# Optimization experiments

Hardware: AMD Instinct MI355X
Metric: run time of the kernel (lower is better)

The kernel has to match this reference:

```python
import jax, jax.numpy as jnp
import numpy as np

B, T, D, K = 4, 2048, 1024, 4

def setup_inputs() -> dict:
    key = jax.random.key(0)
    ks = jax.random.split(key, 4)
    u = jax.random.normal(ks[0], (B, T, D), dtype=jnp.float32)
    s0 = jnp.zeros((B, K, D), dtype=jnp.float32)
    W_in = jax.random.normal(ks[1], (K * D, D), dtype=jnp.float32) * (1.0 / np.sqrt(D))
    b_in = jnp.zeros((K * D,), dtype=jnp.float32)
    W_out = jax.random.normal(ks[2], (D, K * D), dtype=jnp.float32) * (1.0 / np.sqrt(K * D))
    b_out = jnp.zeros((D,), dtype=jnp.float32)
    decay_logit = jax.random.normal(ks[3], (K,), dtype=jnp.float32)
    return {"u": u, "s0": s0, "W_in": W_in, "b_in": b_in,
            "W_out": W_out, "b_out": b_out, "decay_logit": decay_logit}

def reference(u, s0, W_in, b_in, W_out, b_out, decay_logit):
    # u: (B,T,D); s0: (B,K,D)
    Bb, Tt, Dd = u.shape
    Kk = decay_logit.shape[0]
    # input projection -> (B,T,K,D) -> (T,B,K,D) for scan over time
    inp = (jnp.einsum('btd,ed->bte', u, W_in) + b_in).reshape(Bb, Tt, Kk, Dd)
    xs = jnp.transpose(inp, (1, 0, 2, 3))  # (T,B,K,D)
    decay = jax.nn.sigmoid(decay_logit).reshape(1, Kk, 1)  # (1,K,1)

    def step(s, x):
        s_next = decay * s + x
        return s_next, s_next

    s_last, s_seq = jax.lax.scan(step, s0, xs)  # s_seq: (T,B,K,D)
    g_in = jnp.transpose(s_seq, (1, 0, 2, 3)).reshape(Bb, Tt, Kk * Dd)
    g = jnp.einsum('bte,de->btd', g_in, W_out) + b_out
    return g, s_last
```

## Files before the change

kernel.cpp:

```cpp
#include <hip/hip_runtime.h>


#define Bb 4
#define Tt 2048
#define Dd 1024
#define Kk 4
#define BT (Bb*Tt)
#define Ee (Kk*Dd)
#define NCH 32
#define LCH 64

typedef __bf16 bf16x8 __attribute__((ext_vector_type(8)));
typedef float  f32x4  __attribute__((ext_vector_type(4)));

__device__ __forceinline__ float bf2f(ushort u){
  union { unsigned int i; float f; } x; x.i = ((unsigned int)u) << 16; return x.f;
}
__device__ __forceinline__ ushort f2bf(float f){
  union { unsigned int i; float f; } x; x.f = f;
  unsigned int i = x.i;
  return (ushort)((i + 0x7FFFu + ((i >> 16) & 1u)) >> 16);
}
__device__ __forceinline__ float sigm(float x){ return 1.0f / (1.0f + expf(-x)); }

__global__ __launch_bounds__(256) void k_f2bf4(const float4* __restrict__ in,
                                               ushort4* __restrict__ out, int n4){
  int i = blockIdx.x * 256 + threadIdx.x;
  if (i < n4){
    float4 v = in[i];
    ushort4 o; o.x = f2bf(v.x); o.y = f2bf(v.y); o.z = f2bf(v.z); o.w = f2bf(v.w);
    out[i] = o;
  }
}

__global__ __launch_bounds__(256) void k_transpose(const float* __restrict__ in,
                                                   ushort* __restrict__ out){
  __shared__ float tile[32][33];
  int tx = threadIdx.x, ty = threadIdx.y;
  int c0 = blockIdx.x * 32, r0 = blockIdx.y * 32;
  #pragma unroll
  for (int j = 0; j < 4; ++j)
    tile[ty + j*8][tx] = in[(size_t)(r0 + ty + j*8) * Dd + c0 + tx];
  __syncthreads();
  #pragma unroll
  for (int j = 0; j < 4; ++j)
    out[(size_t)(c0 + ty + j*8) * Ee + r0 + tx] = f2bf(tile[tx][ty + j*8]);
}

__global__ __launch_bounds__(256) void gemm_nt(const ushort* __restrict__ A,
                                               const ushort* __restrict__ B,
                                               ushort* __restrict__ C,
                                               int Kred, int lda, int ldb, int ldc,
                                               long aBatch, long bBatch, long cBatch){
  __shared__ ushort As[128 * 32];
  __shared__ ushort Bs[128 * 32];
  A += (long)blockIdx.z * aBatch;
  B += (long)blockIdx.z * bBatch;
  C += (long)blockIdx.z * cBatch;
  const int tid  = threadIdx.x;
  const int lane = tid & 63;
  const int w    = tid >> 6;
  const int wr   = w >> 1, wc = w & 1;
  const int rowBase = blockIdx.x * 128;
  const int colBase = blockIdx.y * 128;

  f32x4 acc[4][4] = {};
  const int krow = (lane >> 4) * 8;
  const int rsel = lane & 15;

  for (int kk = 0; kk < Kred; kk += 32){
    __syncthreads();
    #pragma unroll
    for (int i = 0; i < 2; ++i){
      int c  = i * 256 + tid;
      int r  = c >> 2;
      int c8 = (c & 3) * 8;
      const ushort* ga = A + (size_t)(rowBase + r) * lda + kk + c8;
      const ushort* gb = B + (size_t)(colBase + r) * ldb + kk + c8;
      __builtin_amdgcn_global_load_lds((const __attribute__((address_space(1))) void*)ga,
                                       (__attribute__((address_space(3))) void*)&As[c * 8],
                                       16, 0, 0);
      __builtin_amdgcn_global_load_lds((const __attribute__((address_space(1))) void*)gb,
                                       (__attribute__((address_space(3))) void*)&Bs[c * 8],
                                       16, 0, 0);
    }
    asm volatile("s_waitcnt vmcnt(0)" ::: "memory");
    __syncthreads();

    bf16x8 Af[4], Bf[4];
    #pragma unroll
    for (int mi = 0; mi < 4; ++mi)
      Af[mi] = *(const bf16x8*)&As[(wr*64 + mi*16 + rsel) * 32 + krow];
    #pragma unroll
    for (int ni = 0; ni < 4; ++ni)
      Bf[ni] = *(const bf16x8*)&Bs[(wc*64 + ni*16 + rsel) * 32 + krow];
    #pragma unroll
    for (int mi = 0; mi < 4; ++mi)
      #pragma unroll
      for (int ni = 0; ni < 4; ++ni)
        acc[mi][ni] = __builtin_amdgcn_mfma_f32_16x16x32_bf16(Af[mi], Bf[ni], acc[mi][ni], 0, 0, 0);
  }

  #pragma unroll
  for (int mi = 0; mi < 4; ++mi){
    #pragma unroll
    for (int ni = 0; ni < 4; ++ni){
      int r0 = rowBase + wr*64 + mi*16 + (lane >> 4) * 4;
      int c0 = colBase + wc*64 + ni*16 + (lane & 15);
      #pragma unroll
      for (int q = 0; q < 4; ++q)
        C[(size_t)(r0 + q) * ldc + c0] = f2bf(acc[mi][ni][q]);
    }
  }
}

#define STAGE_HALF(GB, LOFF)                                                   \
  { _Pragma("unroll")                                                          \
    for (int i_ = 0; i_ < 2; ++i_){                                            \
      int c_ = tid + i_*512;                                                   \
      int row_ = c_ >> 2;                                                      \
      int ss_ = (c_ & 3) ^ ((row_ >> 2) & 3);                                  \
      const ushort* g_ = (GB) + (size_t)row_ * 1024 + ss_ * 8;                 \
      __builtin_amdgcn_global_load_lds(                                        \
        (const __attribute__((address_space(1))) void*)g_,                     \
        (__attribute__((address_space(3))) void*)&lds[(LOFF) + c_*8],          \
        16, 0, 0);                                                             \
    } }

#define LDA_FRAGS(KH)                                                          \
  { _Pragma("unroll")                                                          \
    for (int mi_ = 0; mi_ < 8; ++mi_){                                         \
      int r_ = wm*128 + mi_*16 + rsel;                                         \
      int uo_ = r_*32 + kq*8;                                                  \
      uo_ ^= ((uo_ >> 7) & 3) << 3;                                            \
      af[mi_] = *(const bf16x8*)&lds[cbase + (KH)*8192 + uo_];                 \
    } }

#define LDB_FRAGS(KH, NH)                                                      \
  { _Pragma("unroll")                                                          \
    for (int ni_ = 0; ni_ < 2; ++ni_){                                         \
      int r_ = wn*64 + (NH)*32 + ni_*16 + rsel;                                \
      int uo_ = r_*32 + kq*8;                                                  \
      uo_ ^= ((uo_ >> 7) & 3) << 3;                                            \
      bfr[ni_] = *(const bf16x8*)&lds[cbase + 16384 + (KH)*8192 + uo_];        \
    } }

#define MFMA_PH(NH)                                                            \
  { __builtin_amdgcn_s_setprio(1);                                             \
    _Pragma("unroll")                                                          \
    for (int mi_ = 0; mi_ < 8; ++mi_)                                          \
      { _Pragma("unroll")                                                      \
        for (int ni_ = 0; ni_ < 2; ++ni_)                                      \
          acc[mi_][(NH)*2+ni_] = __builtin_amdgcn_mfma_f32_16x16x32_bf16(      \
              af[mi_], bfr[ni_], acc[mi_][(NH)*2+ni_], 0, 0, 0); }             \
    __builtin_amdgcn_s_setprio(0); }

#define BAR() __builtin_amdgcn_s_barrier()

__global__ __launch_bounds__(512, 2) void gemm_big(const ushort* __restrict__ A,
                                                   const ushort* __restrict__ B,
                                                   ushort* __restrict__ C,
                                                   const float* __restrict__ dlog,
                                                   float* __restrict__ carry){
  __shared__ ushort lds[65536];
  const int tid  = threadIdx.x;
  const int lane = tid & 63;
  const int w    = tid >> 6;
  const int wm   = w >> 2;
  const int wn   = w & 3;
  const int rsel = lane & 15;
  const int kq   = lane >> 4;

  int bid = blockIdx.x;
  int xcd = bid & 7, rr = bid >> 3;
  const int rowBase = (((xcd >> 1) << 3) + (rr & 7)) * 256;
  const int colBase = (((xcd & 1) << 3) + (rr >> 3)) * 256;

  const ushort* Ag = A + (size_t)rowBase * 1024;
  const ushort* Bg = B + (size_t)colBase * 1024;

  f32x4 acc[8][4] = {};
  bf16x8 af[8], bfr[2];

  STAGE_HALF(Ag +  0, 0);
  STAGE_HALF(Bg +  0, 16384);
  STAGE_HALF(Ag + 32, 8192);
  STAGE_HALF(Bg + 32, 24576);
  STAGE_HALF(Ag + 64, 32768 + 0);
  STAGE_HALF(Bg + 64, 32768 + 16384);
  STAGE_HALF(Ag + 96, 32768 + 8192);
  asm volatile("s_waitcnt vmcnt(6)" ::: "memory");
  BAR();

  for (int t = 0; t < 16; ++t){
    const int cbase = (t & 1) * 32768;
    const int obase = cbase ^ 32768;
    LDA_FRAGS(0); LDB_FRAGS(0, 0);
    if (t + 1 < 16) STAGE_HALF(Bg + (t+1)*64 + 32, obase + 24576);
    BAR();
    MFMA_PH(0);
    BAR();
    LDB_FRAGS(0, 1);
    if (t + 2 < 16) STAGE_HALF(Ag + (t+2)*64, cbase + 0);
    BAR();
    MFMA_PH(1);
    BAR();
    LDA_FRAGS(1); LDB_FRAGS(1, 0);
    if (t + 2 < 16) STAGE_HALF(Bg + (t+2)*64, cbase + 16384);
    BAR();
    MFMA_PH(0);
    BAR();
    LDB_FRAGS(1, 1);
    if (t + 2 < 16) STAGE_HALF(Ag + (t+2)*64 + 32, cbase + 8192);
    BAR();
    MFMA_PH(1);
    if (t + 2 < 16) { asm volatile("s_waitcnt vmcnt(6)" ::: "memory"); }
    else            { asm volatile("s_waitcnt vmcnt(0)" ::: "memory"); }
    BAR();
  }

  #pragma unroll
  for (int mi = 0; mi < 8; ++mi){
    #pragma unroll
    for (int j = 0; j < 4; ++j){
      #pragma unroll
      for (int q = 0; q < 4; ++q){
        int row = wm*128 + mi*16 + (lane >> 4)*4 + q;
        int col = wn*64 + j*16 + rsel;
        int byte = row*512 + col*2;
        byte ^= ((row >> 2) & 3) << 5;
        *(ushort*)((char*)lds + byte) = f2bf(acc[mi][j][q]);
      }
    }
  }
  __syncthreads();

  {
    const int k_blk = colBase >> 10;
    const int b_blk = rowBase >> 11;
    const int ch0   = (rowBase & 2047) >> 6;
    const int d0    = colBase & 1023;
    const float p   = sigm(dlog[k_blk]);
    #pragma unroll
    for (int s = 0; s < 2; ++s){
      int task = tid + s*512;
      int col = task & 255, ch = task >> 8;
      float a = 0.f;
      for (int i = 0; i < 64; ++i){
        int row = ch*64 + i;
        int byte = row*512 + col*2;
        byte ^= ((row >> 2) & 3) << 5;
        a = p * a + bf2f(*(const ushort*)((char*)lds + byte));
      }
      carry[(size_t)((b_blk*Kk + k_blk)*NCH + ch0 + ch) * Dd + d0 + col] = a;
    }
  }

  #pragma unroll
  for (int j = 0; j < 16; ++j){
    int idx = tid + j*512;
    int r = idx >> 5, c8 = idx & 31;
    int byte = r*512 + c8*16;
    byte ^= ((r >> 2) & 3) << 5;
    f32x4 v = *(const f32x4*)((char*)lds + byte);
    *(f32x4*)&C[(size_t)(rowBase + r) * Ee + colBase + c8*8] = v;
  }
}

__global__ __launch_bounds__(256) void k_z0(const float* __restrict__ Wout,
                                            const float* __restrict__ s0,
                                            float* __restrict__ z0){
  int gid  = blockIdx.x * 4 + (threadIdx.x >> 6);
  int lane = threadIdx.x & 63;
  int d = gid & 1023, k = (gid >> 10) & 3, b = gid >> 12;
  const float* wrow = Wout + (size_t)d * Ee + k * Dd;
  const float* sv   = s0 + ((size_t)(b*Kk + k) << 10);
  float s = 0.f;
  #pragma unroll
  for (int j = 0; j < 16; ++j) s += wrow[lane + j*64] * sv[lane + j*64];
  for (int off = 32; off; off >>= 1) s += __shfl_down(s, off);
  if (lane == 0) z0[gid] = s;
}

__global__ __launch_bounds__(256) void k_cterm(const float* __restrict__ Wout,
                                               const float* __restrict__ b_in,
                                               float* __restrict__ cterm){
  int gid  = blockIdx.x * 4 + (threadIdx.x >> 6);
  int lane = threadIdx.x & 63;
  int d = gid & 1023, k = gid >> 10;
  const float* wrow = Wout + (size_t)d * Ee + k * Dd;
  const float* bv   = b_in + k * Dd;
  float s = 0.f;
  #pragma unroll
  for (int j = 0; j < 16; ++j) s += wrow[lane + j*64] * bv[lane + j*64];
  for (int off = 32; off; off >>= 1) s += __shfl_down(s, off);
  if (lane == 0) cterm[gid] = s;
}

__global__ __launch_bounds__(256) void k_scanInc(const float* __restrict__ carry,
                                                 const float* __restrict__ z0,
                                                 const float* __restrict__ dlog,
                                                 float* __restrict__ incoming){
  int idx = blockIdx.x * 256 + threadIdx.x;
  int k = (idx >> 10) & 3;
  int bk = idx >> 10, d = idx & 1023;
  float p  = sigm(dlog[k]);
  float dL = powf(p, (float)LCH);
  float inc = z0[idx];
  for (int c = 0; c < NCH; ++c){
    size_t o = ((size_t)(bk * NCH + c)) * Dd + d;
    incoming[o] = inc;
    inc = dL * inc + carry[o];
  }
}

__global__ __launch_bounds__(256) void k_scanB(const ushort* __restrict__ Y,
                                               const float* __restrict__ incoming,
                                               const float* __restrict__ dlog,
                                               const float* __restrict__ b_out,
                                               const float* __restrict__ cterm,
                                               float* __restrict__ g){
  int x = blockIdx.x;
  int d = blockIdx.y * 256 + threadIdx.x;
  int c = x & 31, b = x >> 5;
  float p[4], z[4], ct[4], pw[4];
  #pragma unroll
  for (int k = 0; k < 4; ++k){
    p[k]  = sigm(dlog[k]);
    z[k]  = incoming[((size_t)(((b*Kk + k))*NCH + c)) * Dd + d];
    float omp = fmaxf(1.0f - p[k], 1e-30f);
    ct[k] = cterm[k * Dd + d] / omp;
    pw[k] = powf(p[k], (float)(c * LCH + 1));
  }
  float bo = b_out[d];
  size_t ybase = ((size_t)(b*Tt + c*LCH)) * Ee + d;
  size_t gbase = ((size_t)(b*Tt + c*LCH)) * Dd + d;
  for (int i = 0; i < LCH; ++i){
    float acc = bo;
    #pragma unroll
    for (int k = 0; k < 4; ++k){
      z[k] = p[k] * z[k] + bf2f(Y[ybase + (size_t)k * Dd]);
      acc += z[k] + ct[k] * (1.0f - pw[k]);
      pw[k] *= p[k];
    }
    g[gbase] = acc;
    ybase += Ee; gbase += Dd;
  }
}

__global__ __launch_bounds__(256) void k_prep(const float* __restrict__ u,
                                              const float* __restrict__ dlog,
                                              float* __restrict__ vpart,
                                              ushort* __restrict__ U_bf){
  int x = blockIdx.x;
  int d = blockIdx.y * 256 + threadIdx.x;
  int c = x & 31, b = x >> 5;
  float p[4], a[4] = {0.f, 0.f, 0.f, 0.f};
  #pragma unroll
  for (int k = 0; k < 4; ++k) p[k] = sigm(dlog[k]);
  size_t ub = ((size_t)(b*Tt + c*LCH)) * Dd + d;
  for (int i = 0; i < LCH; ++i){
    float uv = u[ub];
    U_bf[ub] = f2bf(uv);
    #pragma unroll
    for (int k = 0; k < 4; ++k) a[k] = p[k] * a[k] + uv;
    ub += Dd;
  }
  #pragma unroll
  for (int k = 0; k < 4; ++k)
    vpart[(((size_t)x) * Kk + k) * Dd + d] = a[k];
}

__global__ __launch_bounds__(256) void k_vcomb(const float* __restrict__ vpart,
                                               const float* __restrict__ dlog,
                                               float* __restrict__ vfull){
  int idx = blockIdx.x * 256 + threadIdx.x;
  int k = (idx >> 10) & 3, b = idx >> 12, d = idx & 1023;
  float p  = sigm(dlog[k]);
  float dL = powf(p, (float)LCH);
  float v = 0.f;
  for (int c = 0; c < NCH; ++c)
    v = dL * v + vpart[(((size_t)(b*NCH + c)) * Kk + k) * Dd + d];
  vfull[idx] = v;
}

__global__ __launch_bounds__(256) void k_slast(const float* __restrict__ W_in,
                                               const float* __restrict__ vfull,
                                               const float* __restrict__ s0,
                                               const float* __restrict__ b_in,
                                               const float* __restrict__ dlog,
                                               float* __restrict__ out){
  int gid  = blockIdx.x * 4 + (threadIdx.x >> 6);
  int lane = threadIdx.x & 63;
  int d = gid & 1023, k = (gid >> 10) & 3, b = gid >> 12;
  const float* wrow = W_in + (size_t)(k*Dd + d) * Dd;
  const float* vv   = vfull + ((size_t)(b*Kk + k) << 10);
  float s = 0.f;
  #pragma unroll
  for (int j = 0; j < 16; ++j) s += wrow[lane + j*64] * vv[lane + j*64];
  for (int off = 32; off; off >>= 1) s += __shfl_down(s, off);
  if (lane == 0){
    float p  = sigm(dlog[k]);
    float pT = powf(p, (float)Tt);
    float omp = 1.0f - p;
    float geo = (omp < 1e-12f) ? (float)Tt : (1.0f - pT) / omp;
    out[gid] = pT * s0[gid] + s + b_in[k*Dd + d] * geo;
  }
}

extern "C" void kernel_launch(void* const* d_in, const int* in_sizes, int n_in,
                              void* d_out, int out_size, void* d_ws, size_t ws_size,
                              hipStream_t stream){
  const float* u     = (const float*)d_in[0];
  const float* s0    = (const float*)d_in[1];
  const float* W_in  = (const float*)d_in[2];
  const float* b_in  = (const float*)d_in[3];
  const float* W_out = (const float*)d_in[4];
  const float* b_out = (const float*)d_in[5];
  const float* dlog  = (const float*)d_in[6];

  float* g_out     = (float*)d_out;
  float* slast_out = g_out + (size_t)BT * Dd;

  char* ws = (char*)d_ws;
  if (ws_size < 115490816ull) return;
  ushort* U_bf    = (ushort*)(ws);
  ushort* WinT    = (ushort*)(ws + 16777216);
  ushort* Wout_bf = (ushort*)(ws + 25165824);
  ushort* Mcat    = (ushort*)(ws + 33554432);
  ushort* Y       = (ushort*)(ws + 41943040);
  float*  carry   = (float*)(ws + 109051904);
  float*  incoming= (float*)(ws + 111149056);
  float*  z0buf   = (float*)(ws + 113246208);
  float*  cterm   = (float*)(ws + 113311744);
  float*  vpart   = (float*)(ws + 113328128);
  float*  vfull   = (float*)(ws + 115425280);

  k_prep<<<dim3(128, 4), 256, 0, stream>>>(u, dlog, vpart, U_bf);
  k_f2bf4<<<4096, 256, 0, stream>>>((const float4*)W_out, (ushort4*)Wout_bf, Dd*Ee/4);
  k_transpose<<<dim3(32, 128), dim3(32, 8), 0, stream>>>(W_in, WinT);

  gemm_nt<<<dim3(8, 8, 4), 256, 0, stream>>>(Wout_bf, WinT, Mcat,
                                             1024, Ee, Ee, Dd,
                                             1024L, 1024L, 1048576L);
  gemm_big<<<512, 512, 0, stream>>>(U_bf, Mcat, Y, dlog, carry);

  k_z0<<<4096, 256, 0, stream>>>(W_out, s0, z0buf);
  k_cterm<<<1024, 256, 0, stream>>>(W_out, b_in, cterm);

  k_scanInc<<<64, 256, 0, stream>>>(carry, z0buf, dlog, incoming);
  k_scanB<<<dim3(128, 4), 256, 0, stream>>>(Y, incoming, dlog, b_out, cterm, g_out);

  k_vcomb<<<64, 256, 0, stream>>>(vpart, dlog, vfull);
  k_slast<<<4096, 256, 0, stream>>>(W_in, vfull, s0, b_in, dlog, slast_out);
}
```

Before: 170.9 us.

## Restructure GEMM main loop into M-half quadrants with tighter prefetch schedule

The big GEMM inner loop now splits work by M halves, loading 4 A fragments and all 4 B fragments per phase instead of 8 A and 2 B. The global-to-LDS prefetch schedule changes so each half-K slice is staged one stage ahead rather than partly two ahead, with explicit lgkmcnt waits and sched barriers before each MFMA block. This aims to cut register pressure and LDS read traffic for A while keeping MFMA issue dense. The cost is less prefetch distance, which may expose more global-load latency, plus extra vmcnt waits.

```diff
diff --git a/kernel.cpp b/kernel.cpp
--- a/kernel.cpp
+++ b/kernel.cpp
@@ -127,32 +127,36 @@
         16, 0, 0);                                                             \
     } }
 
-#define LDA_FRAGS(KH)                                                          \
+#define LDA_H(KH, MH)                                                          \
   { _Pragma("unroll")                                                          \
-    for (int mi_ = 0; mi_ < 8; ++mi_){                                         \
-      int r_ = wm*128 + mi_*16 + rsel;                                         \
+    for (int mi_ = 0; mi_ < 4; ++mi_){                                         \
+      int r_ = wm*128 + (MH)*64 + mi_*16 + rsel;                               \
       int uo_ = r_*32 + kq*8;                                                  \
       uo_ ^= ((uo_ >> 7) & 3) << 3;                                            \
       af[mi_] = *(const bf16x8*)&lds[cbase + (KH)*8192 + uo_];                 \
     } }
 
-#define LDB_FRAGS(KH, NH)                                                      \
+#define LDB_ALL(KH)                                                            \
   { _Pragma("unroll")                                                          \
-    for (int ni_ = 0; ni_ < 2; ++ni_){                                         \
-      int r_ = wn*64 + (NH)*32 + ni_*16 + rsel;                                \
+    for (int ni_ = 0; ni_ < 4; ++ni_){                                         \
+      int r_ = wn*64 + ni_*16 + rsel;                                          \
       int uo_ = r_*32 + kq*8;                                                  \
       uo_ ^= ((uo_ >> 7) & 3) << 3;                                            \
       bfr[ni_] = *(const bf16x8*)&lds[cbase + 16384 + (KH)*8192 + uo_];        \
     } }
 
-#define MFMA_PH(NH)                                                            \
+#define WAIT_LGKM()                                                            \
+  { asm volatile("s_waitcnt lgkmcnt(0)" ::: "memory");                         \
+    __builtin_amdgcn_sched_barrier(0); }
+
+#define MFMA_Q(MH)                                                             \
   { __builtin_amdgcn_s_setprio(1);                                             \
     _Pragma("unroll")                                                          \
-    for (int mi_ = 0; mi_ < 8; ++mi_)                                          \
+    for (int mi_ = 0; mi_ < 4; ++mi_)                                          \
       { _Pragma("unroll")                                                      \
-        for (int ni_ = 0; ni_ < 2; ++ni_)                                      \
-          acc[mi_][(NH)*2+ni_] = __builtin_amdgcn_mfma_f32_16x16x32_bf16(      \
-              af[mi_], bfr[ni_], acc[mi_][(NH)*2+ni_], 0, 0, 0); }             \
+        for (int ni_ = 0; ni_ < 4; ++ni_)                                      \
+          acc[(MH)*4+mi_][ni_] = __builtin_amdgcn_mfma_f32_16x16x32_bf16(      \
+              af[mi_], bfr[ni_], acc[(MH)*4+mi_][ni_], 0, 0, 0); }             \
     __builtin_amdgcn_s_setprio(0); }
 
 #define BAR() __builtin_amdgcn_s_barrier()
@@ -180,7 +184,7 @@
   const ushort* Bg = B + (size_t)colBase * 1024;
 
   f32x4 acc[8][4] = {};
-  bf16x8 af[8], bfr[2];
+  bf16x8 af[4], bfr[4];
 
   STAGE_HALF(Ag +  0, 0);
   STAGE_HALF(Bg +  0, 16384);
@@ -188,34 +192,39 @@
   STAGE_HALF(Bg + 32, 24576);
   STAGE_HALF(Ag + 64, 32768 + 0);
   STAGE_HALF(Bg + 64, 32768 + 16384);
-  STAGE_HALF(Ag + 96, 32768 + 8192);
-  asm volatile("s_waitcnt vmcnt(6)" ::: "memory");
+  asm volatile("s_waitcnt vmcnt(0)" ::: "memory");
   BAR();
 
   for (int t = 0; t < 16; ++t){
     const int cbase = (t & 1) * 32768;
     const int obase = cbase ^ 32768;
-    LDA_FRAGS(0); LDB_FRAGS(0, 0);
-    if (t + 1 < 16) STAGE_HALF(Bg + (t+1)*64 + 32, obase + 24576);
-    BAR();
-    MFMA_PH(0);
-    BAR();
-    LDB_FRAGS(0, 1);
-    if (t + 2 < 16) STAGE_HALF(Ag + (t+2)*64, cbase + 0);
-    BAR();
-    MFMA_PH(1);
-    BAR();
-    LDA_FRAGS(1); LDB_FRAGS(1, 0);
-    if (t + 2 < 16) STAGE_HALF(Bg + (t+2)*64, cbase + 16384);
-    BAR();
-    MFMA_PH(0);
-    BAR();
-    LDB_FRAGS(1, 1);
-    if (t + 2 < 16) STAGE_HALF(Ag + (t+2)*64 + 32, cbase + 8192);
-    BAR();
-    MFMA_PH(1);
-    if (t + 2 < 16) { asm volatile("s_waitcnt vmcnt(6)" ::: "memory"); }
-    else            { asm volatile("s_waitcnt vmcnt(0)" ::: "memory"); }
+    LDA_H(0, 0); LDB_ALL(0);
+    if (t < 15) STAGE_HALF(Ag + (t+1)*64 + 32, obase + 8192);
+    BAR();
+    WAIT_LGKM();
+    MFMA_Q(0);
+    BAR();
+    LDA_H(0, 1);
+    if (t < 15) STAGE_HALF(Bg + (t+1)*64 + 32, obase + 24576);
+    BAR();
+    WAIT_LGKM();
+    MFMA_Q(1);
+    if (t < 15) { asm volatile("s_waitcnt vmcnt(6)" ::: "memory"); }
+    else        { asm volatile("s_waitcnt vmcnt(0)" ::: "memory"); }
+    BAR();
+    LDA_H(1, 0); LDB_ALL(1);
+    if (t < 14) STAGE_HALF(Ag + (t+2)*64, cbase + 0);
+    BAR();
+    WAIT_LGKM();
+    MFMA_Q(0);
+    BAR();
+    LDA_H(1, 1);
+    if (t < 14) STAGE_HALF(Bg + (t+2)*64, cbase + 16384);
+    BAR();
+    WAIT_LGKM();
+    MFMA_Q(1);
+    if (t < 14) { asm volatile("s_waitcnt vmcnt(6)" ::: "memory"); }
+    else        { asm volatile("s_waitcnt vmcnt(0)" ::: "memory"); }
     BAR();
   }
 
```

Result: no change. 170.7 us (-0.1%).
